# Kernel optimization log

Measured on AMD Instinct MI355X. Metric: run time of the kernel, lower is better.

The kernel has to match this reference:

```python
import jax, jax.numpy as jnp
import numpy as np
import math

B, Q, D = 2, 2048, 1024
H, R = 16, 12
DH = D // H
RHO = 2.0
MAX_OFFSET = 6.0


def setup_inputs() -> dict:
    key = jax.random.key(0)
    ks = jax.random.split(key, 16)
    s = 0.02
    inp = {
        'x': jax.random.normal(ks[0], (B, Q, D), dtype=jnp.float32),
        'wq': jax.random.normal(ks[1], (D, D), dtype=jnp.float32) * s,
        'bq': jnp.zeros((D,), jnp.float32),
        'wk': jax.random.normal(ks[2], (D, D), dtype=jnp.float32) * s,
        'bk': jnp.zeros((D,), jnp.float32),
        'wv': jax.random.normal(ks[3], (D, D), dtype=jnp.float32) * s,
        'bv': jnp.zeros((D,), jnp.float32),
        'wo': jax.random.normal(ks[4], (D, D), dtype=jnp.float32) * s,
        'bo': jnp.zeros((D,), jnp.float32),
        'dw_w': jax.random.normal(ks[5], (D, 1, 3), dtype=jnp.float32) * s,  # depthwise conv1d k=3
        'dw_b': jnp.zeros((D,), jnp.float32),
        'pw_w': jax.random.normal(ks[6], (H * R, D), dtype=jnp.float32) * s,  # pointwise conv1d k=1
        'pw_b': jnp.zeros((H * R,), jnp.float32),
        'rel_scale': jnp.asarray(0.1, jnp.float32),
    }
    return inp


def _split_heads(y):
    b, q, d = y.shape
    return y.reshape(b, q, H, DH).transpose(0, 2, 1, 3)  # (b,h,q,dh)


def _sample(seq, pos):
    # seq: (b,h,q,dh), pos: (b,h,q,r) fractional positions -> (b,h,q,r,dh)
    b, h, q, dh = seq.shape
    low = jnp.clip(jnp.floor(pos), 0, q - 1).astype(jnp.int32)
    high = jnp.clip(jnp.ceil(pos), 0, q - 1).astype(jnp.int32)
    frac = (pos - low.astype(pos.dtype))[..., None]
    bi = jnp.arange(b)[:, None, None, None]
    hi = jnp.arange(h)[None, :, None, None]
    gl = seq[bi, hi, low]   # (b,h,q,r,dh) gather
    gh = seq[bi, hi, high]
    return gl * (1.0 - frac) + gh * frac


def reference(x, wq, bq, wk, bk, wv, bv, wo, bo, dw_w, dw_b, pw_w, pw_b, rel_scale):
    b, q, d = x.shape
    q_lin = x @ wq.T + bq
    qh = _split_heads(q_lin)
    kh = _split_heads(x @ wk.T + bk)
    vh = _split_heads(x @ wv.T + bv)

    # learned offsets: depthwise conv (k=3, groups=d) -> gelu -> pointwise conv
    feat = q_lin.transpose(0, 2, 1)  # (b,d,q)
    dw = jax.lax.conv_general_dilated(
        feat, dw_w, window_strides=(1,), padding=[(1, 1)],
        feature_group_count=D, dimension_numbers=('NCH', 'OIH', 'NCH'))
    dw = dw + dw_b[None, :, None]
    g = jax.nn.gelu(dw, approximate=False)
    off = jnp.einsum('od,bdq->boq', pw_w, g) + pw_b[None, :, None]  # (b,h*r,q)
    off = off.transpose(0, 2, 1).reshape(b, q, H, R).transpose(0, 2, 1, 3)  # (b,h,q,r)
    off = jnp.tanh(off) * MAX_OFFSET

    base = jnp.arange(q, dtype=x.dtype)[None, None, :, None]
    anchor = jnp.linspace(-RHO, RHO, R, dtype=x.dtype)[None, None, None, :]
    positions = jnp.clip(base + anchor + off, 0.0, q - 1.0)  # (b,h,q,r)

    sk = _sample(kh, positions)  # (b,h,q,r,dh)
    sv = _sample(vh, positions)

    scores = jnp.einsum('bhqd,bhqrd->bhqr', qh, sk) / math.sqrt(DH)
    rel = positions - jnp.arange(q, dtype=x.dtype)[None, None, :, None]
    scores = scores - rel_scale * jnp.abs(rel)
    attn = jax.nn.softmax(scores, axis=-1)
    out = jnp.einsum('bhqr,bhqrd->bhqd', attn, sv)  # (b,h,q,dh)
    out = out.transpose(0, 2, 1, 3).reshape(b, q, d)
    return out @ wo.T + bo
```

## Files before the change

kernel.cpp:

```cpp
#include <hip/hip_runtime.h>
#include <math.h>

constexpr int B_  = 2;
constexpr int Q_  = 2048;
constexpr int D_  = 1024;
constexpr int H_  = 16;
constexpr int R_  = 12;
constexpr int DH_ = 64;
constexpr int M_  = B_ * Q_;
constexpr int HR_ = H_ * R_;
constexpr int NQKV = 3 * D_;

typedef short bf16x8 __attribute__((ext_vector_type(8)));
typedef float f32x4  __attribute__((ext_vector_type(4)));

__device__ __forceinline__ float bf2f(unsigned short u) {
    return __uint_as_float(((unsigned)u) << 16);
}
__device__ __forceinline__ unsigned short f2bf(float f) {
    unsigned u = __float_as_uint(f);
    return (unsigned short)((u + 0x7fffu + ((u >> 16) & 1u)) >> 16);
}

__global__ __launch_bounds__(256) void cvt_all(const float* __restrict__ x,
                                               const float* __restrict__ wq,
                                               const float* __restrict__ wk,
                                               const float* __restrict__ wv,
                                               const float* __restrict__ wo,
                                               const float* __restrict__ pww,
                                               const float* __restrict__ bq,
                                               const float* __restrict__ bk,
                                               const float* __restrict__ bv,
                                               unsigned short* __restrict__ xb,
                                               unsigned short* __restrict__ wqkv,
                                               unsigned short* __restrict__ wob,
                                               unsigned short* __restrict__ pwwb,
                                               float* __restrict__ bqkv) {
    const int blk = blockIdx.x;
    if (blk >= 4192) {
        const int i = (blk - 4192) * 256 + threadIdx.x;
        bqkv[i] = i < D_ ? bq[i] : (i < 2 * D_ ? bk[i - D_] : bv[i - 2 * D_]);
        return;
    }
    const int i = blk * 256 + threadIdx.x;
    const float* src;
    unsigned short* dst;
    int rel;
    if (i < 524288)       { src = x;   dst = xb;                          rel = i; }
    else if (i < 655360)  { src = wq;  dst = wqkv;                        rel = i - 524288; }
    else if (i < 786432)  { src = wk;  dst = wqkv + (size_t)D_ * D_;      rel = i - 655360; }
    else if (i < 917504)  { src = wv;  dst = wqkv + (size_t)2 * D_ * D_;  rel = i - 786432; }
    else if (i < 1048576) { src = wo;  dst = wob;                         rel = i - 917504; }
    else                  { src = pww; dst = pwwb;                        rel = i - 1048576; }

    const float4 a = ((const float4*)src)[2 * rel];
    const float4 b = ((const float4*)src)[2 * rel + 1];
    uint4 o;
    o.x = (unsigned)f2bf(a.x) | ((unsigned)f2bf(a.y) << 16);
    o.y = (unsigned)f2bf(a.z) | ((unsigned)f2bf(a.w) << 16);
    o.z = (unsigned)f2bf(b.x) | ((unsigned)f2bf(b.y) << 16);
    o.w = (unsigned)f2bf(b.z) | ((unsigned)f2bf(b.w) << 16);
    ((uint4*)dst)[rel] = o;
}

template <int BN, bool OUT_BF16>
__global__ __launch_bounds__(256) void gemm_mfma(const unsigned short* __restrict__ A,
                                                 const unsigned short* __restrict__ W,
                                                 const float* __restrict__ bias,
                                                 void* __restrict__ Cv,
                                                 int M, int N, int K) {
    constexpr int BM  = 128, BK = 64;
    constexpr int FN  = BN / 32;
    constexpr int CHA = BM / 8;
    constexpr int CHB = BN / 8;
    __shared__ unsigned short As[BM * BK];
    __shared__ unsigned short Bs[BN * BK];

    const int tid  = threadIdx.x;
    const int w    = tid >> 6, lane = tid & 63;
    const int wm   = w >> 1,   wn   = w & 1;

    const int nbx = gridDim.x;
    const int nwg = nbx * gridDim.y;
    int flat = blockIdx.y * nbx + blockIdx.x;
    flat = (flat & 7) * (nwg >> 3) + (flat >> 3);
    const int bm = (flat / nbx) * BM;
    const int bn = (flat % nbx) * BN;

    const int srow  = lane >> 3;
    const int sslot = (lane & 7) ^ (srow & 7);
    const int fr = lane & 15;
    const int s  = lane >> 4;
    const int fx = fr & 7;

    f32x4 acc[4][FN];
    #pragma unroll
    for (int i = 0; i < 4; ++i)
        #pragma unroll
        for (int j = 0; j < FN; ++j) acc[i][j] = (f32x4){0.f, 0.f, 0.f, 0.f};

    for (int k0 = 0; k0 < K; k0 += BK) {
        __syncthreads();
        #pragma unroll
        for (int c = w; c < CHA; c += 4) {
            const unsigned short* g = A + (size_t)(bm + c * 8 + srow) * K + k0 + sslot * 8;
            __builtin_amdgcn_global_load_lds(
                (const __attribute__((address_space(1))) void*)g,
                (__attribute__((address_space(3))) void*)((char*)As + c * 1024), 16, 0, 0);
        }
        #pragma unroll
        for (int c = w; c < CHB; c += 4) {
            const unsigned short* g = W + (size_t)(bn + c * 8 + srow) * K + k0 + sslot * 8;
            __builtin_amdgcn_global_load_lds(
                (const __attribute__((address_space(1))) void*)g,
                (__attribute__((address_space(3))) void*)((char*)Bs + c * 1024), 16, 0, 0);
        }
        __syncthreads();

        #pragma unroll
        for (int ks = 0; ks < 2; ++ks) {
            const int sl = (((ks << 2) | s) ^ fx) * 8;
            bf16x8 af[4];
            #pragma unroll
            for (int i = 0; i < 4; ++i)
                af[i] = *(const bf16x8*)(As + (wm * 64 + i * 16 + fr) * BK + sl);
            #pragma unroll
            for (int j = 0; j < FN; ++j) {
                const bf16x8 bfrag = *(const bf16x8*)(Bs + (wn * (BN / 2) + j * 16 + fr) * BK + sl);
                #pragma unroll
                for (int i = 0; i < 4; ++i)
                    acc[i][j] = __builtin_amdgcn_mfma_f32_16x16x32_bf16(af[i], bfrag, acc[i][j], 0, 0, 0);
            }
        }
    }

    #pragma unroll
    for (int j = 0; j < FN; ++j) {
        const int col = bn + wn * (BN / 2) + j * 16 + fr;
        const float bv = bias[col];
        #pragma unroll
        for (int i = 0; i < 4; ++i) {
            const int row0 = bm + wm * 64 + i * 16 + ((lane >> 4) << 2);
            #pragma unroll
            for (int ii = 0; ii < 4; ++ii) {
                const float v = acc[i][j][ii] + bv;
                if constexpr (OUT_BF16)
                    ((unsigned short*)Cv)[(size_t)(row0 + ii) * N + col] = f2bf(v);
                else
                    ((float*)Cv)[(size_t)(row0 + ii) * N + col] = v;
            }
        }
    }
}

__global__ __launch_bounds__(256) void dwgelu_kernel(const unsigned short* __restrict__ qkv,
                                                     const float* __restrict__ dww,
                                                     const float* __restrict__ dwb,
                                                     unsigned short* __restrict__ g) {
    const int idx = blockIdx.x * 256 + threadIdx.x;
    const int m   = idx >> 7;
    const int c8  = (idx & 127) << 3;
    const int t   = m & (Q_ - 1);
    const unsigned short* row = qkv + (size_t)m * NQKV + c8;

    unsigned short cur[8], prv[8] = {0}, nxt[8] = {0};
    *(uint4*)cur = *(const uint4*)row;
    if (t > 0)      *(uint4*)prv = *(const uint4*)(row - NQKV);
    if (t < Q_ - 1) *(uint4*)nxt = *(const uint4*)(row + NQKV);

    float dwl[24];
    #pragma unroll
    for (int q2 = 0; q2 < 6; ++q2)
        *(f32x4*)&dwl[q2 * 4] = *(const f32x4*)&dww[c8 * 3 + q2 * 4];
    float db[8];
    *(f32x4*)&db[0] = *(const f32x4*)&dwb[c8];
    *(f32x4*)&db[4] = *(const f32x4*)&dwb[c8 + 4];

    unsigned short o[8];
    #pragma unroll
    for (int j = 0; j < 8; ++j) {
        float v = bf2f(prv[j]) * dwl[j * 3 + 0] + bf2f(cur[j]) * dwl[j * 3 + 1]
                + bf2f(nxt[j]) * dwl[j * 3 + 2] + db[j];
        v = 0.5f * v * (1.0f + erff(v * 0.70710678118654752f));
        o[j] = f2bf(v);
    }
    *(uint4*)(g + (size_t)m * D_ + c8) = *(uint4*)o;
}

__global__ __launch_bounds__(256) void coeff_pv_kernel(const unsigned short* __restrict__ qkv,
                                                       const unsigned short* __restrict__ offb,
                                                       const float* __restrict__ rel_scale_p,
                                                       unsigned short* __restrict__ attb) {
    __shared__ __align__(16) float S[4][16][33];
    __shared__ __align__(16) float C[4][16][32];
    const int tid  = threadIdx.x;
    const int w    = tid >> 6, lane = tid & 63;
    const int tile = blockIdx.x * 4 + w;
    const int t0   = (tile & 127) << 4;
    const int h    = (tile >> 7) & 15;
    const int b    = tile >> 11;
    const int fr   = lane & 15;
    const int fo   = (lane >> 4) << 3;

    const unsigned short* qrow = qkv + (size_t)(b * Q_ + t0 + fr) * NQKV + h * DH_ + fo;
    const bf16x8 af0 = *(const bf16x8*)qrow;
    const bf16x8 af1 = *(const bf16x8*)(qrow + 32);

    f32x4 acc0 = (f32x4){0.f, 0.f, 0.f, 0.f};
    f32x4 acc1 = acc0;
    {
        int j = min(max(t0 - 8 + fr, 0), Q_ - 1);
        const unsigned short* krow = qkv + (size_t)(b * Q_ + j) * NQKV + D_ + h * DH_ + fo;
        acc0 = __builtin_amdgcn_mfma_f32_16x16x32_bf16(af0, *(const bf16x8*)krow, acc0, 0, 0, 0);
        acc0 = __builtin_amdgcn_mfma_f32_16x16x32_bf16(af1, *(const bf16x8*)(krow + 32), acc0, 0, 0, 0);
    }
    {
        int j = min(max(t0 + 8 + fr, 0), Q_ - 1);
        const unsigned short* krow = qkv + (size_t)(b * Q_ + j) * NQKV + D_ + h * DH_ + fo;
        acc1 = __builtin_amdgcn_mfma_f32_16x16x32_bf16(af0, *(const bf16x8*)krow, acc1, 0, 0, 0);
        acc1 = __builtin_amdgcn_mfma_f32_16x16x32_bf16(af1, *(const bf16x8*)(krow + 32), acc1, 0, 0, 0);
    }

    float vj[32];
    {
        const unsigned short* vb = qkv + (size_t)b * Q_ * NQKV + 2 * D_ + h * DH_ + lane;
        #pragma unroll
        for (int i2 = 0; i2 < 32; ++i2) {
            const int j = min(max(t0 - 8 + i2, 0), Q_ - 1);
            vj[i2] = bf2f(vb[(size_t)j * NQKV]);
        }
    }

    const int row0 = (lane >> 4) << 2;
    #pragma unroll
    for (int ii = 0; ii < 4; ++ii) {
        S[w][row0 + ii][fr]      = acc0[ii];
        S[w][row0 + ii][16 + fr] = acc1[ii];
    }
    {
        const int tr = lane >> 2, cg = (lane & 3) << 3;
        #pragma unroll
        for (int k = 0; k < 8; ++k) C[w][tr][cg + k] = 0.f;
    }
    __syncthreads();

    const int tloc = lane & 15;
    const int rs   = lane >> 4;
    const int t    = t0 + tloc;
    const float rel_scale = rel_scale_p[0];
    const unsigned short* offrow = offb + (size_t)(b * Q_ + t) * HR_ + h * R_;

    float sc[3], fr3[3];
    int   cl[3], ch[3];
    #pragma unroll
    for (int i = 0; i < 3; ++i) {
        const int r = rs * 3 + i;
        const float off    = bf2f(offrow[r]);
        const float anchor = -2.0f + (4.0f / 11.0f) * (float)r;
        float pos = (float)t + anchor + 6.0f * tanhf(off);
        pos = fminf(fmaxf(pos, 0.0f), (float)(Q_ - 1));
        const float fl = floorf(pos);
        const int lo = (int)fl;
        const int hi = (int)ceilf(pos);
        const float f = pos - fl;
        cl[i] = lo - t0 + 8;
        ch[i] = hi - t0 + 8;
        fr3[i] = f;
        const float slo = S[w][tloc][cl[i]];
        const float shi = S[w][tloc][ch[i]];
        sc[i] = (slo * (1.0f - f) + shi * f) * 0.125f - rel_scale * fabsf(pos - (float)t);
    }

    float mx = fmaxf(fmaxf(sc[0], sc[1]), sc[2]);
    mx = fmaxf(mx, __shfl_xor(mx, 16));
    mx = fmaxf(mx, __shfl_xor(mx, 32));
    float e[3];
    #pragma unroll
    for (int i = 0; i < 3; ++i) e[i] = expf(sc[i] - mx);
    float sum = e[0] + e[1] + e[2];
    sum += __shfl_xor(sum, 16);
    sum += __shfl_xor(sum, 32);
    const float inv = 1.0f / sum;

    #pragma unroll
    for (int i = 0; i < 3; ++i) {
        const float wgt = e[i] * inv;
        atomicAdd(&C[w][tloc][cl[i]], wgt * (1.0f - fr3[i]));
        atomicAdd(&C[w][tloc][ch[i]], wgt * fr3[i]);
    }
    __syncthreads();

    #pragma unroll
    for (int tl = 0; tl < 16; ++tl) {
        const int st = tl & ~3;
        float cw[20];
        #pragma unroll
        for (int q2 = 0; q2 < 5; ++q2)
            *(f32x4*)&cw[q2 * 4] = *(const f32x4*)&C[w][tl][st + q2 * 4];
        float acc2 = 0.f;
        #pragma unroll
        for (int k = 0; k <= 16; ++k)
            acc2 = fmaf(cw[tl - st + k], vj[tl + k], acc2);
        attb[(size_t)(b * Q_ + t0 + tl) * D_ + h * DH_ + lane] = f2bf(acc2);
    }
}

extern "C" void kernel_launch(void* const* d_in, const int* in_sizes, int n_in,
                              void* d_out, int out_size, void* d_ws, size_t ws_size,
                              hipStream_t stream) {
    const float* x    = (const float*)d_in[0];
    const float* wq   = (const float*)d_in[1];
    const float* bq   = (const float*)d_in[2];
    const float* wk   = (const float*)d_in[3];
    const float* bk   = (const float*)d_in[4];
    const float* wv   = (const float*)d_in[5];
    const float* bv   = (const float*)d_in[6];
    const float* wo   = (const float*)d_in[7];
    const float* bo   = (const float*)d_in[8];
    const float* dww  = (const float*)d_in[9];
    const float* dwb  = (const float*)d_in[10];
    const float* pww  = (const float*)d_in[11];
    const float* pwb  = (const float*)d_in[12];
    const float* rsc  = (const float*)d_in[13];
    float* out = (float*)d_out;

    unsigned short* xb   = (unsigned short*)d_ws;
    unsigned short* wqkv = xb   + (size_t)M_ * D_;
    unsigned short* wob  = wqkv + (size_t)NQKV * D_;
    unsigned short* pwwb = wob  + (size_t)D_ * D_;
    unsigned short* qkv  = pwwb + (size_t)HR_ * D_;
    unsigned short* gb   = qkv  + (size_t)M_ * NQKV;
    unsigned short* offb = gb   + (size_t)M_ * D_;
    unsigned short* attb = offb + (size_t)M_ * HR_;
    float*          bqkv = (float*)(attb + (size_t)M_ * D_);

    dim3 blk(256);

    hipLaunchKernelGGL(cvt_all, dim3(4204), blk, 0, stream,
                       x, wq, wk, wv, wo, pww, bq, bk, bv, xb, wqkv, wob, pwwb, bqkv);

    hipLaunchKernelGGL((gemm_mfma<128, true>), dim3(NQKV / 128, M_ / 128), blk, 0, stream,
                       xb, wqkv, bqkv, qkv, M_, NQKV, D_);

    hipLaunchKernelGGL(dwgelu_kernel, dim3(M_ * 128 / 256), blk, 0, stream, qkv, dww, dwb, gb);

    hipLaunchKernelGGL((gemm_mfma<64, true>), dim3(HR_ / 64, M_ / 128), blk, 0, stream,
                       gb, pwwb, pwb, offb, M_, HR_, D_);

    hipLaunchKernelGGL(coeff_pv_kernel, dim3(B_ * H_ * (Q_ / 16) / 4), blk, 0, stream,
                       qkv, offb, rsc, attb);

    hipLaunchKernelGGL((gemm_mfma<64, false>), dim3(D_ / 64, M_ / 128), blk, 0, stream,
                       attb, wob, bo, out, M_, D_, D_);
}
```

Baseline: 97.73 us.

## Fuse depthwise conv+GELU into pointwise offset GEMM; widen output GEMM tile

Replaces the separate dwgelu kernel and the small pointwise GEMM with one kernel. Each block computes the conv+GELU result for 16 rows into XOR-swizzled LDS and multiplies it against all 192 pointwise weights with MFMA, streaming the weights through LDS with global_load_lds. This removes the round-trip of the g intermediate through global memory and one launch, but every one of the 256 blocks rereads the full pointwise weight matrix. The output projection GEMM also moves from a 64-wide to a 128-wide N tile, which halves its grid.

```diff
diff --git a/kernel.cpp b/kernel.cpp
--- a/kernel.cpp
+++ b/kernel.cpp
@@ -153,38 +153,94 @@
     }
 }
 
-__global__ __launch_bounds__(256) void dwgelu_kernel(const unsigned short* __restrict__ qkv,
-                                                     const float* __restrict__ dww,
-                                                     const float* __restrict__ dwb,
-                                                     unsigned short* __restrict__ g) {
-    const int idx = blockIdx.x * 256 + threadIdx.x;
-    const int m   = idx >> 7;
-    const int c8  = (idx & 127) << 3;
-    const int t   = m & (Q_ - 1);
-    const unsigned short* row = qkv + (size_t)m * NQKV + c8;
-
-    unsigned short cur[8], prv[8] = {0}, nxt[8] = {0};
-    *(uint4*)cur = *(const uint4*)row;
-    if (t > 0)      *(uint4*)prv = *(const uint4*)(row - NQKV);
-    if (t < Q_ - 1) *(uint4*)nxt = *(const uint4*)(row + NQKV);
-
-    float dwl[24];
-    #pragma unroll
-    for (int q2 = 0; q2 < 6; ++q2)
-        *(f32x4*)&dwl[q2 * 4] = *(const f32x4*)&dww[c8 * 3 + q2 * 4];
-    float db[8];
-    *(f32x4*)&db[0] = *(const f32x4*)&dwb[c8];
-    *(f32x4*)&db[4] = *(const f32x4*)&dwb[c8 + 4];
-
-    unsigned short o[8];
-    #pragma unroll
-    for (int j = 0; j < 8; ++j) {
-        float v = bf2f(prv[j]) * dwl[j * 3 + 0] + bf2f(cur[j]) * dwl[j * 3 + 1]
-                + bf2f(nxt[j]) * dwl[j * 3 + 2] + db[j];
-        v = 0.5f * v * (1.0f + erff(v * 0.70710678118654752f));
-        o[j] = f2bf(v);
-    }
-    *(uint4*)(g + (size_t)m * D_ + c8) = *(uint4*)o;
+__global__ __launch_bounds__(256) void dwpw_kernel(const unsigned short* __restrict__ qkv,
+                                                   const float* __restrict__ dww,
+                                                   const float* __restrict__ dwb,
+                                                   const unsigned short* __restrict__ pwwb,
+                                                   const float* __restrict__ pwb,
+                                                   unsigned short* __restrict__ offb) {
+    __shared__ unsigned short As[16 * 1024];
+    __shared__ unsigned short Bs[192 * 64];
+    const int tid  = threadIdx.x;
+    const int w    = tid >> 6, lane = tid & 63;
+    const int m0   = blockIdx.x * 16;
+
+    for (int u = tid; u < 16 * 128; u += 256) {
+        const int r  = u >> 7;
+        const int c8 = (u & 127) << 3;
+        const int m  = m0 + r;
+        const int t  = m & (Q_ - 1);
+        const unsigned short* row = qkv + (size_t)m * NQKV + c8;
+
+        unsigned short cur[8], prv[8] = {0}, nxt[8] = {0};
+        *(uint4*)cur = *(const uint4*)row;
+        if (t > 0)      *(uint4*)prv = *(const uint4*)(row - NQKV);
+        if (t < Q_ - 1) *(uint4*)nxt = *(const uint4*)(row + NQKV);
+
+        float dwl[24];
+        #pragma unroll
+        for (int q2 = 0; q2 < 6; ++q2)
+            *(f32x4*)&dwl[q2 * 4] = *(const f32x4*)&dww[c8 * 3 + q2 * 4];
+        float db[8];
+        *(f32x4*)&db[0] = *(const f32x4*)&dwb[c8];
+        *(f32x4*)&db[4] = *(const f32x4*)&dwb[c8 + 4];
+
+        unsigned short o[8];
+        #pragma unroll
+        for (int j = 0; j < 8; ++j) {
+            float v = bf2f(prv[j]) * dwl[j * 3 + 0] + bf2f(cur[j]) * dwl[j * 3 + 1]
+                    + bf2f(nxt[j]) * dwl[j * 3 + 2] + db[j];
+            v = 0.5f * v * (1.0f + erff(v * 0.70710678118654752f));
+            o[j] = f2bf(v);
+        }
+        const int slot = (c8 >> 3) ^ (r & 7);
+        *(uint4*)(As + r * 1024 + slot * 8) = *(uint4*)o;
+    }
+    __syncthreads();
+
+    const int srow  = lane >> 3;
+    const int sslot = (lane & 7) ^ (srow & 7);
+    const int fr = lane & 15;
+    const int s  = lane >> 4;
+    const int fx = fr & 7;
+
+    f32x4 acc[3];
+    #pragma unroll
+    for (int j = 0; j < 3; ++j) acc[j] = (f32x4){0.f, 0.f, 0.f, 0.f};
+
+    for (int k0 = 0; k0 < 1024; k0 += 64) {
+        if (k0) __syncthreads();
+        #pragma unroll
+        for (int c = w; c < 24; c += 4) {
+            const unsigned short* g = pwwb + (size_t)(c * 8 + srow) * 1024 + k0 + sslot * 8;
+            __builtin_amdgcn_global_load_lds(
+                (const __attribute__((address_space(1))) void*)g,
+                (__attribute__((address_space(3))) void*)((char*)Bs + c * 1024), 16, 0, 0);
+        }
+        __syncthreads();
+
+        #pragma unroll
+        for (int ks = 0; ks < 2; ++ks) {
+            const int aslot = ((k0 >> 3) + ((ks << 2) | s)) ^ fx;
+            const bf16x8 af = *(const bf16x8*)(As + fr * 1024 + aslot * 8);
+            const int sl = (((ks << 2) | s) ^ fx) * 8;
+            #pragma unroll
+            for (int j = 0; j < 3; ++j) {
+                const bf16x8 bfrag = *(const bf16x8*)(Bs + (w * 48 + j * 16 + fr) * 64 + sl);
+                acc[j] = __builtin_amdgcn_mfma_f32_16x16x32_bf16(af, bfrag, acc[j], 0, 0, 0);
+            }
+        }
+    }
+
+    #pragma unroll
+    for (int j = 0; j < 3; ++j) {
+        const int n = w * 48 + j * 16 + fr;
+        const float bv = pwb[n];
+        const int row0 = (lane >> 4) << 2;
+        #pragma unroll
+        for (int ii = 0; ii < 4; ++ii)
+            offb[(size_t)(m0 + row0 + ii) * HR_ + n] = f2bf(acc[j][ii] + bv);
+    }
 }
 
 __global__ __launch_bounds__(256) void coeff_pv_kernel(const unsigned short* __restrict__ qkv,
@@ -329,8 +385,7 @@
     unsigned short* wob  = wqkv + (size_t)NQKV * D_;
     unsigned short* pwwb = wob  + (size_t)D_ * D_;
     unsigned short* qkv  = pwwb + (size_t)HR_ * D_;
-    unsigned short* gb   = qkv  + (size_t)M_ * NQKV;
-    unsigned short* offb = gb   + (size_t)M_ * D_;
+    unsigned short* offb = qkv  + (size_t)M_ * NQKV;
     unsigned short* attb = offb + (size_t)M_ * HR_;
     float*          bqkv = (float*)(attb + (size_t)M_ * D_);
 
@@ -342,14 +397,12 @@
     hipLaunchKernelGGL((gemm_mfma<128, true>), dim3(NQKV / 128, M_ / 128), blk, 0, stream,
                        xb, wqkv, bqkv, qkv, M_, NQKV, D_);
 
-    hipLaunchKernelGGL(dwgelu_kernel, dim3(M_ * 128 / 256), blk, 0, stream, qkv, dww, dwb, gb);
-
-    hipLaunchKernelGGL((gemm_mfma<64, true>), dim3(HR_ / 64, M_ / 128), blk, 0, stream,
-                       gb, pwwb, pwb, offb, M_, HR_, D_);
+    hipLaunchKernelGGL(dwpw_kernel, dim3(M_ / 16), blk, 0, stream,
+                       qkv, dww, dwb, pwwb, pwb, offb);
 
     hipLaunchKernelGGL(coeff_pv_kernel, dim3(B_ * H_ * (Q_ / 16) / 4), blk, 0, stream,
                        qkv, offb, rsc, attb);
 
-    hipLaunchKernelGGL((gemm_mfma<64, false>), dim3(D_ / 64, M_ / 128), blk, 0, stream,
+    hipLaunchKernelGGL((gemm_mfma<128, false>), dim3(D_ / 128, M_ / 128), blk, 0, stream,
                        attb, wob, bo, out, M_, D_, D_);
 }
```

After: 101.7 us. +4.0%, slower.
